# Kernel optimization log

Measured on AMD Instinct MI355X. Metric: run time of the kernel, lower is better.

Reference implementation:

```python
import jax, jax.numpy as jnp
import numpy as np
from jax import lax

B, C, H, W = 2, 256, 64, 64
KC, RD = C // 8, C // 16  # key_channels=32, GatherExcite rd_channels=16
EPS = 1e-5


def setup_inputs() -> dict:
    key = jax.random.key(0)
    ks = jax.random.split(key, 17)
    s = 0.05
    n = lambda k, shp: jax.random.normal(k, shp, jnp.float32) * s
    return {
        "x": jax.random.normal(ks[0], (B, C, H, W), jnp.float32),
        "Wq": n(ks[1], (KC, C)),
        "Wk": n(ks[2], (KC, C)),
        "Wv": n(ks[3], (C, C)),
        "Wb1": n(ks[4], (KC, C)),
        "Wb2": n(ks[5], (KC, C)),
        "w_gb": jax.random.normal(ks[6], (), jnp.float32),  # 1x1 conv on 1-channel bias map
        "ge_w1": n(ks[7], (RD, C)),
        "ge_b1": jnp.zeros((RD,), jnp.float32),
        "ge_w2": n(ks[8], (C, RD)),
        "ge_b2": jnp.zeros((C,), jnp.float32),
        "Wo": n(ks[9], (C, C)),
        "bn_scale": jnp.ones((C,), jnp.float32),
        "bn_bias": jnp.zeros((C,), jnp.float32),
        "bn_mean": jax.random.normal(ks[10], (C,), jnp.float32) * 0.01,
        "bn_var": jnp.ones((C,), jnp.float32),
        "gamma": jax.random.normal(ks[11], (), jnp.float32) * 0.1,
    }


def _conv1x1(t, w):  # t: [B,Cin,H,W], w: [Cout,Cin]
    return jnp.einsum('bchw,oc->bohw', t, w)


def reference(x, Wq, Wk, Wv, Wb1, Wb2, w_gb, ge_w1, ge_b1, ge_w2, ge_b2,
              Wo, bn_scale, bn_bias, bn_mean, bn_var, gamma):
    b, c, h, w = x.shape
    hw = h * w

    # GatherExcite (extent=0, use_mlp=True, gate=sigmoid): global mean -> ConvMlp -> sigmoid gate
    m = x.mean(axis=(2, 3), keepdims=True)                     # [B,C,1,1]
    g = jax.nn.relu(_conv1x1(m, ge_w1) + ge_b1[None, :, None, None])
    g = _conv1x1(g, ge_w2) + ge_b2[None, :, None, None]
    key_in = x * jax.nn.sigmoid(g)                             # [B,C,H,W]

    value = _conv1x1(x, Wv).reshape(b, c, hw).transpose(0, 2, 1)   # [B,HW,C]
    query = _conv1x1(x, Wq).reshape(b, KC, hw).transpose(0, 2, 1)  # [B,HW,Kc]
    key_f = _conv1x1(key_in, Wk).reshape(b, KC, hw)                # [B,Kc,HW]

    sim = jnp.einsum('bnk,bkm->bnm', query, key_f)                 # [B,HW,HW]

    # bias branch (dropout is identity at eval)
    b1 = jax.nn.relu(_conv1x1(x, Wb1)).reshape(b, KC, hw)          # [B,Kc,HW]
    b2 = jax.nn.relu(_conv1x1(x, Wb2)).reshape(b, KC, hw)          # [B,Kc,HW]
    bias = jnp.einsum('bkn,bkm->bnm', b1, b2)                      # [B,HW,HW]

    # AvgPool2d(k=3, s=1, pad=1, count_include_pad=True) on [B,1,HW,HW]
    pooled = lax.reduce_window(bias[:, None], 0.0, lax.add,
                               (1, 1, 3, 3), (1, 1, 1, 1),
                               [(0, 0), (0, 0), (1, 1), (1, 1)]) / 9.0
    bias_map = jax.nn.sigmoid(w_gb * pooled)[:, 0]                 # [B,HW,HW]

    attn = jax.nn.softmax(sim * bias_map, axis=-1)                 # [B,HW,HW]
    ctx = jnp.einsum('bnm,bmc->bnc', attn, value)                  # [B,HW,C]
    ctx = ctx.transpose(0, 2, 1).reshape(b, c, h, w)

    # W: conv1x1 -> BatchNorm (inference) -> ReLU
    y = _conv1x1(ctx, Wo)
    y = (y - bn_mean[None, :, None, None]) * (bn_scale / jnp.sqrt(bn_var + EPS))[None, :, None, None] \
        + bn_bias[None, :, None, None]
    y = jax.nn.relu(y)

    return gamma * y + x
```

## Files before the change

### kernel.cpp

```cpp
#include <hip/hip_runtime.h>
#include <hip/hip_bf16.h>

typedef __bf16 bf16;
typedef __bf16 v8bf __attribute__((ext_vector_type(8)));
typedef __bf16 v4bf __attribute__((ext_vector_type(4)));
typedef float v4f __attribute__((ext_vector_type(4)));

#define HW 4096
#define CH 256
#define KC 32
#define RD 16
#define NB 2
#define BNEPS 1e-5f
#define VSTRIDE 4224
#define LOG2E 1.4426950408889634f

__device__ __forceinline__ float fexp2(float x) {
#if __has_builtin(__builtin_amdgcn_exp2f)
  return __builtin_amdgcn_exp2f(x);
#else
  return exp2f(x);
#endif
}
__device__ __forceinline__ float frcp(float x) {
#if __has_builtin(__builtin_amdgcn_rcpf)
  return __builtin_amdgcn_rcpf(x);
#else
  return 1.f / x;
#endif
}

#define OFF_QT     0u
#define OFF_KT     524288u
#define OFF_BS1    1048576u
#define OFF_BS2    1572864u
#define OFF_VT     2097152u
#define OFF_B1R    6422528u
#define OFF_B2R    6946816u
#define OFF_PACC   7471104u
#define OFF_PL     41025536u
#define OFF_WOBF   41287680u
#define OFF_XBT    41418752u
#define OFF_WALL   45613056u
#define OFF_MPART  46006272u

__global__ __launch_bounds__(256) void k_prep(const float* __restrict__ x,
    bf16* __restrict__ xbt, float* __restrict__ mpart) {
  __shared__ __align__(16) float ts[64][68];
  const int blk = blockIdx.x;
  const int b  = blk >> 8;
  const int id = blk & 255;
  const int ct = id >> 6, nt = id & 63;
  const int c0 = ct * 64, n0 = nt * 64;
  const int t = threadIdx.x;
  const int crow = t >> 2, nch = (t & 3) * 16;
  const float* xp = x + ((size_t)(b * CH + c0 + crow)) * HW + n0 + nch;
  #pragma unroll
  for (int i = 0; i < 4; ++i)
    *(v4f*)&ts[crow][nch + i * 4] = *(const v4f*)(xp + i * 4);
  __syncthreads();
  {
    float p = 0.f;
    #pragma unroll
    for (int j = 0; j < 16; ++j) p += ts[crow][nch + j];
    p += __shfl_xor(p, 1);
    p += __shfl_xor(p, 2);
    if ((t & 3) == 0) mpart[(size_t)(b * CH + c0 + crow) * 64 + nt] = p;
  }
  const int nl = t >> 2, cc0 = (t & 3) * 16;
  bf16* dst = xbt + ((size_t)(b * HW + n0 + nl)) * CH + c0 + cc0;
  v8bf o0, o1;
  #pragma unroll
  for (int j = 0; j < 8; ++j) { o0[j] = (bf16)ts[cc0 + j][nl]; o1[j] = (bf16)ts[cc0 + 8 + j][nl]; }
  *(v8bf*)dst = o0;
  *(v8bf*)(dst + 8) = o1;
}

__global__ __launch_bounds__(256) void k_pack(
    const float* __restrict__ mpart,
    const float* __restrict__ gw1, const float* __restrict__ gb1,
    const float* __restrict__ gw2, const float* __restrict__ gb2,
    const float* __restrict__ Wq, const float* __restrict__ Wk,
    const float* __restrict__ Wb1, const float* __restrict__ Wb2,
    const float* __restrict__ Wv, const float* __restrict__ Wo,
    bf16* __restrict__ wall, bf16* __restrict__ wo_bf) {
  __shared__ float ms[CH];
  __shared__ float hid[RD];
  const int blk = blockIdx.x;
  const int t = threadIdx.x;
  if (blk >= 768) {
    int i = (blk - 768) * 256 + t;
    wo_bf[i] = (bf16)Wo[i];
    return;
  }
  const int b = blk / 384, row = blk % 384;
  float v;
  if (row < 32)       v = Wq[row * CH + t] * LOG2E;
  else if (row < 64) {
    float m = 0.f;
    const float* mp = mpart + (size_t)(b * CH + t) * 64;
    #pragma unroll
    for (int j = 0; j < 64; ++j) m += mp[j];
    ms[t] = m * (1.0f / HW);
    __syncthreads();
    if (t < RD) {
      float a = gb1[t];
      for (int c = 0; c < CH; ++c) a += gw1[t * CH + c] * ms[c];
      hid[t] = fmaxf(a, 0.f);
    }
    __syncthreads();
    float a = gb2[t];
    #pragma unroll
    for (int r = 0; r < RD; ++r) a += gw2[t * RD + r] * hid[r];
    float s = 1.f / (1.f + __expf(-a));
    v = Wk[(row - 32) * CH + t] * s;
  }
  else if (row < 96)  v = Wb1[(row - 64) * CH + t];
  else if (row < 128) v = Wb2[(row - 96) * CH + t];
  else                v = Wv[(row - 128) * CH + t];
  wall[((size_t)b * 384 + row) * CH + t] = (bf16)v;
}

__global__ __launch_bounds__(256, 4) void k_proj(
    const bf16* __restrict__ xbt, const bf16* __restrict__ wall,
    bf16* __restrict__ qt, bf16* __restrict__ kt,
    bf16* __restrict__ b1r, bf16* __restrict__ b2r, bf16* __restrict__ vt) {
  __shared__ __align__(16) bf16 xs[32][264];
  __shared__ __align__(16) bf16 tr[4][16][24];
  const int blk = blockIdx.x;
  const int b  = blk >> 9;
  const int bm = (blk >> 7) & 3;
  const int nt = blk & 127;
  const int n0 = nt * 32;
  const int t = threadIdx.x;
  {
    const int row = t >> 3, c0 = (t & 7) * 32;
    const bf16* src = xbt + ((size_t)(b * HW + n0 + row)) * CH + c0;
    #pragma unroll
    for (int i = 0; i < 4; ++i)
      *(v8bf*)&xs[row][c0 + i * 8] = *(const v8bf*)(src + i * 8);
  }
  __syncthreads();
  const int w = t >> 6, lane = t & 63, cl = lane & 15, kh = lane >> 4;
  const int nsub = (w & 1) * 16;
  const int otrio = (w >> 1) * 3;
  const v4f vzero = {0.f, 0.f, 0.f, 0.f};
  v4f acc[3] = {vzero, vzero, vzero};
  const bf16* wb = wall + ((size_t)b * 384 + bm * 96) * CH;
  for (int kk = 0; kk < 8; ++kk) {
    v8bf bx = *(const v8bf*)&xs[nsub + cl][kk * 32 + kh * 8];
    #pragma unroll
    for (int j = 0; j < 3; ++j) {
      v8bf af = *(const v8bf*)(wb + (size_t)((otrio + j) * 16 + cl) * CH + kk * 32 + kh * 8);
      acc[j] = __builtin_amdgcn_mfma_f32_16x16x32_bf16(af, bx, acc[j], 0, 0, 0);
    }
  }
  const int n = n0 + nsub + cl;
  #pragma unroll
  for (int j = 0; j < 3; ++j) {
    const int o0 = bm * 96 + (otrio + j) * 16;
    if (o0 < 128) {
      const bool rel = (o0 >= 64);
      v4bf pk;
      #pragma unroll
      for (int r = 0; r < 4; ++r) {
        float v = acc[j][r];
        if (rel) v = fmaxf(v, 0.f);
        pk[r] = (bf16)v;
      }
      const int seg = o0 >> 5;
      bf16* base = seg == 0 ? qt : seg == 1 ? kt : seg == 2 ? b1r : b2r;
      *(v4bf*)&base[((size_t)b * HW + n) * KC + (o0 & 31) + kh * 4] = pk;
    } else {
      #pragma unroll
      for (int r = 0; r < 4; ++r) tr[w][kh * 4 + r][cl] = (bf16)acc[j][r];
      asm volatile("s_waitcnt lgkmcnt(0)" ::: "memory");
      __builtin_amdgcn_sched_barrier(0);
      const int row = lane >> 2, nch = (lane & 3) * 4;
      v4bf d = *(const v4bf*)&tr[w][row][nch];
      *(v4bf*)&vt[((size_t)b * CH + (o0 - 128) + row) * VSTRIDE + n0 + nsub + nch] = d;
    }
  }
}

__global__ __launch_bounds__(256) void k_pool(const bf16* __restrict__ b1r,
    const bf16* __restrict__ b2r, const float* __restrict__ wgb,
    bf16* __restrict__ bs1, bf16* __restrict__ bs2) {
  int i = blockIdx.x * 256 + threadIdx.x;
  int n = (i >> 5) & (HW - 1);
  float a = (float)b1r[i], c = (float)b2r[i];
  if (n > 0)      { a += (float)b1r[i - KC]; c += (float)b2r[i - KC]; }
  if (n < HW - 1) { a += (float)b1r[i + KC]; c += (float)b2r[i + KC]; }
  const float ws = -LOG2E * wgb[0] * (1.f / 9.f);
  bs1[i] = (bf16)(a * ws);
  bs2[i] = (bf16)c;
}

__global__ __launch_bounds__(256, 4) void k_attn(
    const bf16* __restrict__ qtg, const bf16* __restrict__ ktg,
    const bf16* __restrict__ bs1g, const bf16* __restrict__ bs2g,
    const bf16* __restrict__ vtg,
    bf16* __restrict__ pacc, float* __restrict__ pl) {
  __shared__ __align__(16) bf16 vbuf[128][64];
  __shared__ __align__(16) bf16 kbuf[2][32][40];
  __shared__ __align__(16) bf16 bbuf[2][32][40];
  __shared__ __align__(16) bf16 plds[2][64][40];
  const int blk = blockIdx.x;
  const int rt  = blk >> 3;
  const int os  = blk & 7;
  const int b   = rt >> 6;
  const int row0 = (rt & 63) * 64;
  const int t = threadIdx.x;
  const int w = t >> 6;
  const int lane = t & 63;
  const int cl = lane & 15, kh = lane >> 4;
  const int kb = os * 512;
  const v4f vzero = {0.f, 0.f, 0.f, 0.f};
  const size_t qoff = ((size_t)(b * HW + row0 + w * 16 + cl)) * KC + kh * 8;
  const v8bf qf  = *(const v8bf*)(qtg + qoff);
  const v8bf b1f = *(const v8bf*)(bs1g + qoff);
  const bf16* kt = ktg + (size_t)b * HW * KC;
  const bf16* b2 = bs2g + (size_t)b * HW * KC;
  const bf16* vt = vtg + (size_t)b * CH * VSTRIDE;
  const int sr = (t >> 2) & 31, sl = (t & 3) * 8;
  const bf16* sbase = (t < 128) ? kt : b2;
  bf16* sd0 = (t < 128) ? &kbuf[0][sr][sl] : &bbuf[0][sr][sl];
  bf16* sd1 = (t < 128) ? &kbuf[1][sr][sl] : &bbuf[1][sr][sl];
  const int vsl = lane & 3;
  const int vslot3 = ((((lane >> 2) & 1) * 4 + vsl) ^ (lane >> 3)) * 8;
  const int rline = w * 32 + (cl >> 1);
  const int rslot = ((((cl & 1) * 4) + kh) ^ (cl >> 1)) * 8;

  *(v8bf*)sd0 = *(const v8bf*)(sbase + (size_t)(kb + sr) * KC + sl);
  __syncthreads();

  v4f acc[16];
  #pragma unroll
  for (int f = 0; f < 16; ++f) acc[f] = vzero;
  float psum = 0.f;

  for (int s = 0; s < 16; ++s) {
    const int m0 = kb + s * 32;
    const int pb = s & 1;
    v8bf vr[4];
    #pragma unroll
    for (int i = 0; i < 4; ++i)
      vr[i] = *(const v8bf*)(vt + (size_t)(w * 64 + i * 16 + (lane >> 2)) * VSTRIDE + m0 + vsl * 8);
    v8bf pr;
    if (s < 15)
      pr = *(const v8bf*)(sbase + (size_t)(m0 + 32 + sr) * KC + sl);
    #pragma unroll
    for (int cb = 0; cb < 2; ++cb) {
      v8bf kf  = *(const v8bf*)&kbuf[pb][cb * 16 + cl][kh * 8];
      v8bf b2f = *(const v8bf*)&bbuf[pb][cb * 16 + cl][kh * 8];
      v4f sim = __builtin_amdgcn_mfma_f32_16x16x32_bf16(kf,  qf,  vzero, 0, 0, 0);
      v4f bia = __builtin_amdgcn_mfma_f32_16x16x32_bf16(b2f, b1f, vzero, 0, 0, 0);
      v4bf pk;
      #pragma unroll
      for (int r = 0; r < 4; ++r) {
        float bm = frcp(1.f + fexp2(bia[r]));
        float pv = fexp2(sim[r] * bm);
        psum += pv;
        pk[r] = (bf16)pv;
      }
      *(v4bf*)&plds[pb][w * 16 + cl][cb * 16 + kh * 4] = pk;
    }
    #pragma unroll
    for (int i = 0; i < 4; ++i)
      *(v8bf*)&vbuf[w * 32 + i * 8 + (lane >> 3)][vslot3] = vr[i];
    if (s < 15) {
      bf16* sd = pb ? sd0 : sd1;
      *(v8bf*)sd = pr;
    }
    __syncthreads();
    v8bf vf[4], pa[4];
    #pragma unroll
    for (int f = 0; f < 4; ++f)
      vf[f] = *(const v8bf*)&vbuf[rline + f * 8][rslot];
    #pragma unroll
    for (int rg = 0; rg < 4; ++rg)
      pa[rg] = *(const v8bf*)&plds[pb][rg * 16 + cl][kh * 8];
    #pragma unroll
    for (int rg = 0; rg < 4; ++rg)
      #pragma unroll
      for (int f = 0; f < 4; ++f)
        acc[rg * 4 + f] = __builtin_amdgcn_mfma_f32_16x16x32_bf16(pa[rg], vf[f], acc[rg * 4 + f], 0, 0, 0);
  }
  __syncthreads();

  {
    float s2 = psum;
    s2 += __shfl_xor(s2, 16);
    s2 += __shfl_xor(s2, 32);
    if (kh == 0) pl[blk * 64 + w * 16 + cl] = s2;
  }
  bf16 (*ep)[64] = (bf16 (*)[64])vbuf;
  bf16* po = pacc + (size_t)blk * 64 * CH;
  for (int rg = 0; rg < 4; ++rg) {
    #pragma unroll
    for (int f = 0; f < 4; ++f)
      #pragma unroll
      for (int r = 0; r < 4; ++r)
        ep[w * 16 + kh * 4 + r][f * 16 + cl] = (bf16)acc[rg * 4 + f][r];
    asm volatile("s_waitcnt lgkmcnt(0)" ::: "memory");
    __builtin_amdgcn_sched_barrier(0);
    #pragma unroll
    for (int it = 0; it < 2; ++it) {
      int row = lane >> 2, chunk = it * 4 + (lane & 3);
      v8bf d = *(const v8bf*)&ep[w * 16 + row][chunk * 8];
      *(v8bf*)&po[(size_t)(rg * 16 + row) * CH + w * 64 + chunk * 8] = d;
    }
  }
}

__global__ __launch_bounds__(256) void k_outc(
    const bf16* __restrict__ pacc, const float* __restrict__ pl,
    const bf16* __restrict__ wo,
    const float* __restrict__ bns, const float* __restrict__ bnb,
    const float* __restrict__ bnm, const float* __restrict__ bnv,
    const float* __restrict__ gamma, const float* __restrict__ x,
    float* __restrict__ out) {
  __shared__ __align__(16) bf16 cs[16][264];
  const int blk = blockIdx.x;
  const int n0g = blk * 16;
  const int b   = n0g >> 12;
  const int n0  = n0g & (HW - 1);
  const int t = threadIdx.x;
  const int base = (blk >> 2) * 8;
  {
    const int r16 = t >> 4;
    const int ch0 = (t & 15) * 16;
    const int rl = (blk & 3) * 16 + r16;
    float den = 0.f;
    #pragma unroll
    for (int s = 0; s < 8; ++s) den += pl[(base + s) * 64 + rl];
    const float inv = 1.f / den;
    float sum[16];
    #pragma unroll
    for (int j = 0; j < 16; ++j) sum[j] = 0.f;
    #pragma unroll
    for (int s = 0; s < 8; ++s) {
      const bf16* pp = &pacc[((size_t)(base + s) * 64 + rl) * CH + ch0];
      v8bf p0 = *(const v8bf*)pp;
      v8bf p1 = *(const v8bf*)(pp + 8);
      #pragma unroll
      for (int j = 0; j < 8; ++j) { sum[j] += (float)p0[j]; sum[8 + j] += (float)p1[j]; }
    }
    v8bf o0, o1;
    #pragma unroll
    for (int j = 0; j < 8; ++j) {
      o0[j] = (bf16)(sum[j] * inv);
      o1[j] = (bf16)(sum[8 + j] * inv);
    }
    *(v8bf*)&cs[r16][ch0] = o0;
    *(v8bf*)&cs[r16][ch0 + 8] = o1;
  }
  __syncthreads();
  const int w = t >> 6, lane = t & 63, cl = lane & 15, kh = lane >> 4;
  const v4f vzero = {0.f, 0.f, 0.f, 0.f};
  v8bf a[8];
  #pragma unroll
  for (int kk = 0; kk < 8; ++kk)
    a[kk] = *(const v8bf*)&cs[cl][kk * 32 + kh * 8];
  v4f acc[4] = {vzero, vzero, vzero, vzero};
  #pragma unroll
  for (int kk = 0; kk < 8; ++kk)
    #pragma unroll
    for (int cg = 0; cg < 4; ++cg) {
      v8bf bfr = *(const v8bf*)(wo + (size_t)(w * 64 + cg * 16 + cl) * CH + kk * 32 + kh * 8);
      acc[cg] = __builtin_amdgcn_mfma_f32_16x16x32_bf16(a[kk], bfr, acc[cg], 0, 0, 0);
    }
  const float g = gamma[0];
  #pragma unroll
  for (int cg = 0; cg < 4; ++cg) {
    int o = w * 64 + cg * 16 + cl;
    float isc = bns[o] / sqrtf(bnv[o] + BNEPS);
    float mu = bnm[o], bb = bnb[o];
    size_t oi = ((size_t)b * CH + o) * HW + n0 + kh * 4;
    v4f xv = *(const v4f*)&x[oi];
    v4f ov;
    #pragma unroll
    for (int r = 0; r < 4; ++r) {
      float v = (acc[cg][r] - mu) * isc + bb;
      v = fmaxf(v, 0.f);
      ov[r] = g * v + xv[r];
    }
    *(v4f*)&out[oi] = ov;
  }
}

extern "C" void kernel_launch(void* const* d_in, const int* in_sizes, int n_in,
                              void* d_out, int out_size, void* d_ws, size_t ws_size,
                              hipStream_t stream) {
  const float* x    = (const float*)d_in[0];
  const float* Wq   = (const float*)d_in[1];
  const float* Wk   = (const float*)d_in[2];
  const float* Wv   = (const float*)d_in[3];
  const float* Wb1  = (const float*)d_in[4];
  const float* Wb2  = (const float*)d_in[5];
  const float* wgb  = (const float*)d_in[6];
  const float* gw1  = (const float*)d_in[7];
  const float* gb1  = (const float*)d_in[8];
  const float* gw2  = (const float*)d_in[9];
  const float* gb2  = (const float*)d_in[10];
  const float* Wo   = (const float*)d_in[11];
  const float* bns  = (const float*)d_in[12];
  const float* bnb  = (const float*)d_in[13];
  const float* bnm  = (const float*)d_in[14];
  const float* bnv  = (const float*)d_in[15];
  const float* gam  = (const float*)d_in[16];

  char* ws = (char*)d_ws;
  bf16* qt    = (bf16*)(ws + OFF_QT);
  bf16* kt    = (bf16*)(ws + OFF_KT);
  bf16* bs1   = (bf16*)(ws + OFF_BS1);
  bf16* bs2   = (bf16*)(ws + OFF_BS2);
  bf16* vt    = (bf16*)(ws + OFF_VT);
  bf16* b1r   = (bf16*)(ws + OFF_B1R);
  bf16* b2r   = (bf16*)(ws + OFF_B2R);
  bf16* pacc  = (bf16*)(ws + OFF_PACC);
  float* plv  = (float*)(ws + OFF_PL);
  bf16* wobf  = (bf16*)(ws + OFF_WOBF);
  bf16* xbt   = (bf16*)(ws + OFF_XBT);
  bf16* wall  = (bf16*)(ws + OFF_WALL);
  float* mprt = (float*)(ws + OFF_MPART);
  float* out  = (float*)d_out;

  hipLaunchKernelGGL(k_prep, dim3(512),  dim3(256), 0, stream, x, xbt, mprt);
  hipLaunchKernelGGL(k_pack, dim3(1024), dim3(256), 0, stream, mprt, gw1, gb1, gw2, gb2,
                     Wq, Wk, Wb1, Wb2, Wv, Wo, wall, wobf);
  hipLaunchKernelGGL(k_proj, dim3(1024), dim3(256), 0, stream, xbt, wall, qt, kt, b1r, b2r, vt);
  hipLaunchKernelGGL(k_pool, dim3(NB * HW * KC / 256), dim3(256), 0, stream, b1r, b2r, wgb, bs1, bs2);
  hipLaunchKernelGGL(k_attn, dim3(1024), dim3(256), 0, stream, qt, kt, bs1, bs2, vt, pacc, plv);
  hipLaunchKernelGGL(k_outc, dim3(512),  dim3(256), 0, stream, pacc, plv, wobf, bns, bnb, bnm, bnv, gam, x, out);
}
```

Baseline: 88.19 us.

## Fuse bias pooling into projection and attention loads, prefetch V one step ahead

Removes the separate k_pool kernel. The w_gb scale is folded into the b1 projection epilogue, and the 3-tap row sums of b1/b2 are computed on the fly while loading into the attention kernel. The attention loop now register-prefetches the next V tile and the next K/B tiles a full iteration ahead, uses a lighter barrier macro, and raises wave priority around the MFMA block. This saves a kernel launch and a global round trip, at the cost of extra redundant loads and adds inside the attention kernel, plus more register pressure.

```diff
diff --git a/kernel.cpp b/kernel.cpp
--- a/kernel.cpp
+++ b/kernel.cpp
@@ -30,12 +30,16 @@
 #endif
 }
 
+#define BLOCK_SYNC() do {                                   \
+  asm volatile("s_waitcnt lgkmcnt(0)" ::: "memory");        \
+  __builtin_amdgcn_s_barrier();                             \
+  __builtin_amdgcn_sched_barrier(0);                        \
+} while (0)
+
 #define OFF_QT     0u
 #define OFF_KT     524288u
-#define OFF_BS1    1048576u
-#define OFF_BS2    1572864u
 #define OFF_VT     2097152u
-#define OFF_B1R    6422528u
+#define OFF_B1S    6422528u
 #define OFF_B2R    6946816u
 #define OFF_PACC   7471104u
 #define OFF_PL     41025536u
@@ -123,8 +127,9 @@
 
 __global__ __launch_bounds__(256, 4) void k_proj(
     const bf16* __restrict__ xbt, const bf16* __restrict__ wall,
+    const float* __restrict__ wgb,
     bf16* __restrict__ qt, bf16* __restrict__ kt,
-    bf16* __restrict__ b1r, bf16* __restrict__ b2r, bf16* __restrict__ vt) {
+    bf16* __restrict__ b1s, bf16* __restrict__ b2r, bf16* __restrict__ vt) {
   __shared__ __align__(16) bf16 xs[32][264];
   __shared__ __align__(16) bf16 tr[4][16][24];
   const int blk = blockIdx.x;
@@ -155,21 +160,22 @@
       acc[j] = __builtin_amdgcn_mfma_f32_16x16x32_bf16(af, bx, acc[j], 0, 0, 0);
     }
   }
+  const float ws = -LOG2E * wgb[0] * (1.f / 9.f);
   const int n = n0 + nsub + cl;
   #pragma unroll
   for (int j = 0; j < 3; ++j) {
     const int o0 = bm * 96 + (otrio + j) * 16;
     if (o0 < 128) {
-      const bool rel = (o0 >= 64);
+      const int seg = o0 >> 5;
       v4bf pk;
       #pragma unroll
       for (int r = 0; r < 4; ++r) {
         float v = acc[j][r];
-        if (rel) v = fmaxf(v, 0.f);
+        if (seg == 2)      v = ws * fmaxf(v, 0.f);
+        else if (seg == 3) v = fmaxf(v, 0.f);
         pk[r] = (bf16)v;
       }
-      const int seg = o0 >> 5;
-      bf16* base = seg == 0 ? qt : seg == 1 ? kt : seg == 2 ? b1r : b2r;
+      bf16* base = seg == 0 ? qt : seg == 1 ? kt : seg == 2 ? b1s : b2r;
       *(v4bf*)&base[((size_t)b * HW + n) * KC + (o0 & 31) + kh * 4] = pk;
     } else {
       #pragma unroll
@@ -183,22 +189,9 @@
   }
 }
 
-__global__ __launch_bounds__(256) void k_pool(const bf16* __restrict__ b1r,
-    const bf16* __restrict__ b2r, const float* __restrict__ wgb,
-    bf16* __restrict__ bs1, bf16* __restrict__ bs2) {
-  int i = blockIdx.x * 256 + threadIdx.x;
-  int n = (i >> 5) & (HW - 1);
-  float a = (float)b1r[i], c = (float)b2r[i];
-  if (n > 0)      { a += (float)b1r[i - KC]; c += (float)b2r[i - KC]; }
-  if (n < HW - 1) { a += (float)b1r[i + KC]; c += (float)b2r[i + KC]; }
-  const float ws = -LOG2E * wgb[0] * (1.f / 9.f);
-  bs1[i] = (bf16)(a * ws);
-  bs2[i] = (bf16)c;
-}
-
 __global__ __launch_bounds__(256, 4) void k_attn(
     const bf16* __restrict__ qtg, const bf16* __restrict__ ktg,
-    const bf16* __restrict__ bs1g, const bf16* __restrict__ bs2g,
+    const bf16* __restrict__ b1sg, const bf16* __restrict__ b2rg,
     const bf16* __restrict__ vtg,
     bf16* __restrict__ pacc, float* __restrict__ pl) {
   __shared__ __align__(16) bf16 vbuf[128][64];
@@ -216,22 +209,53 @@
   const int cl = lane & 15, kh = lane >> 4;
   const int kb = os * 512;
   const v4f vzero = {0.f, 0.f, 0.f, 0.f};
-  const size_t qoff = ((size_t)(b * HW + row0 + w * 16 + cl)) * KC + kh * 8;
-  const v8bf qf  = *(const v8bf*)(qtg + qoff);
-  const v8bf b1f = *(const v8bf*)(bs1g + qoff);
   const bf16* kt = ktg + (size_t)b * HW * KC;
-  const bf16* b2 = bs2g + (size_t)b * HW * KC;
+  const bf16* b2 = b2rg + (size_t)b * HW * KC;
   const bf16* vt = vtg + (size_t)b * CH * VSTRIDE;
+  const int qrow = row0 + w * 16 + cl;
+  const v8bf qf = *(const v8bf*)(qtg + ((size_t)(b * HW + qrow)) * KC + kh * 8);
+  v8bf b1f;
+  {
+    const bf16* bp = b1sg + (size_t)b * HW * KC;
+    v8bf c0 = *(const v8bf*)(bp + (size_t)qrow * KC + kh * 8);
+    v8bf cm = *(const v8bf*)(bp + (size_t)(qrow > 0 ? qrow - 1 : 0) * KC + kh * 8);
+    v8bf cp = *(const v8bf*)(bp + (size_t)(qrow < HW - 1 ? qrow + 1 : HW - 1) * KC + kh * 8);
+    #pragma unroll
+    for (int j = 0; j < 8; ++j) {
+      float sv = (float)c0[j];
+      if (qrow > 0)      sv += (float)cm[j];
+      if (qrow < HW - 1) sv += (float)cp[j];
+      b1f[j] = (bf16)sv;
+    }
+  }
   const int sr = (t >> 2) & 31, sl = (t & 3) * 8;
-  const bf16* sbase = (t < 128) ? kt : b2;
-  bf16* sd0 = (t < 128) ? &kbuf[0][sr][sl] : &bbuf[0][sr][sl];
-  bf16* sd1 = (t < 128) ? &kbuf[1][sr][sl] : &bbuf[1][sr][sl];
+  const bool isK = (t < 128);
   const int vsl = lane & 3;
   const int vslot3 = ((((lane >> 2) & 1) * 4 + vsl) ^ (lane >> 3)) * 8;
   const int rline = w * 32 + (cl >> 1);
   const int rslot = ((((cl & 1) * 4) + kh) ^ (cl >> 1)) * 8;
 
-  *(v8bf*)sd0 = *(const v8bf*)(sbase + (size_t)(kb + sr) * KC + sl);
+  if (isK) {
+    *(v8bf*)&kbuf[0][sr][sl] = *(const v8bf*)(kt + (size_t)(kb + sr) * KC + sl);
+  } else {
+    int g = kb + sr;
+    v8bf c0 = *(const v8bf*)(b2 + (size_t)g * KC + sl);
+    v8bf cm = *(const v8bf*)(b2 + (size_t)(g > 0 ? g - 1 : 0) * KC + sl);
+    v8bf cp = *(const v8bf*)(b2 + (size_t)(g < HW - 1 ? g + 1 : HW - 1) * KC + sl);
+    v8bf o;
+    #pragma unroll
+    for (int j = 0; j < 8; ++j) {
+      float sv = (float)c0[j];
+      if (g > 0)      sv += (float)cm[j];
+      if (g < HW - 1) sv += (float)cp[j];
+      o[j] = (bf16)sv;
+    }
+    *(v8bf*)&bbuf[0][sr][sl] = o;
+  }
+  v8bf vcur[4];
+  #pragma unroll
+  for (int i = 0; i < 4; ++i)
+    vcur[i] = *(const v8bf*)(vt + (size_t)(w * 64 + i * 16 + (lane >> 2)) * VSTRIDE + kb + vsl * 8);
   __syncthreads();
 
   v4f acc[16];
@@ -239,16 +263,24 @@
   for (int f = 0; f < 16; ++f) acc[f] = vzero;
   float psum = 0.f;
 
+  #pragma unroll 2
   for (int s = 0; s < 16; ++s) {
     const int m0 = kb + s * 32;
     const int pb = s & 1;
-    v8bf vr[4];
-    #pragma unroll
-    for (int i = 0; i < 4; ++i)
-      vr[i] = *(const v8bf*)(vt + (size_t)(w * 64 + i * 16 + (lane >> 2)) * VSTRIDE + m0 + vsl * 8);
-    v8bf pr;
-    if (s < 15)
-      pr = *(const v8bf*)(sbase + (size_t)(m0 + 32 + sr) * KC + sl);
+    v8bf kr0, br0, br1, br2, vn[4];
+    if (s < 15) {
+      const int g = m0 + 32 + sr;
+      if (isK) {
+        kr0 = *(const v8bf*)(kt + (size_t)g * KC + sl);
+      } else {
+        br1 = *(const v8bf*)(b2 + (size_t)g * KC + sl);
+        br0 = *(const v8bf*)(b2 + (size_t)(g - 1) * KC + sl);
+        br2 = *(const v8bf*)(b2 + (size_t)(g < HW - 1 ? g + 1 : HW - 1) * KC + sl);
+      }
+      #pragma unroll
+      for (int i = 0; i < 4; ++i)
+        vn[i] = *(const v8bf*)(vt + (size_t)(w * 64 + i * 16 + (lane >> 2)) * VSTRIDE + m0 + 32 + vsl * 8);
+    }
     #pragma unroll
     for (int cb = 0; cb < 2; ++cb) {
       v8bf kf  = *(const v8bf*)&kbuf[pb][cb * 16 + cl][kh * 8];
@@ -265,14 +297,25 @@
       }
       *(v4bf*)&plds[pb][w * 16 + cl][cb * 16 + kh * 4] = pk;
     }
+    if (s < 15) {
+      if (isK) {
+        *(v8bf*)&kbuf[pb ^ 1][sr][sl] = kr0;
+      } else {
+        const int g = m0 + 32 + sr;
+        v8bf o;
+        #pragma unroll
+        for (int j = 0; j < 8; ++j) {
+          float sv = (float)br1[j] + (float)br0[j];
+          if (g < HW - 1) sv += (float)br2[j];
+          o[j] = (bf16)sv;
+        }
+        *(v8bf*)&bbuf[pb ^ 1][sr][sl] = o;
+      }
+    }
     #pragma unroll
     for (int i = 0; i < 4; ++i)
-      *(v8bf*)&vbuf[w * 32 + i * 8 + (lane >> 3)][vslot3] = vr[i];
-    if (s < 15) {
-      bf16* sd = pb ? sd0 : sd1;
-      *(v8bf*)sd = pr;
-    }
-    __syncthreads();
+      *(v8bf*)&vbuf[w * 32 + i * 8 + (lane >> 3)][vslot3] = vcur[i];
+    BLOCK_SYNC();
     v8bf vf[4], pa[4];
     #pragma unroll
     for (int f = 0; f < 4; ++f)
@@ -280,11 +323,17 @@
     #pragma unroll
     for (int rg = 0; rg < 4; ++rg)
       pa[rg] = *(const v8bf*)&plds[pb][rg * 16 + cl][kh * 8];
+    __builtin_amdgcn_s_setprio(1);
     #pragma unroll
     for (int rg = 0; rg < 4; ++rg)
       #pragma unroll
       for (int f = 0; f < 4; ++f)
         acc[rg * 4 + f] = __builtin_amdgcn_mfma_f32_16x16x32_bf16(pa[rg], vf[f], acc[rg * 4 + f], 0, 0, 0);
+    __builtin_amdgcn_s_setprio(0);
+    if (s < 15) {
+      #pragma unroll
+      for (int i = 0; i < 4; ++i) vcur[i] = vn[i];
+    }
   }
   __syncthreads();
 
@@ -413,10 +462,8 @@
   char* ws = (char*)d_ws;
   bf16* qt    = (bf16*)(ws + OFF_QT);
   bf16* kt    = (bf16*)(ws + OFF_KT);
-  bf16* bs1   = (bf16*)(ws + OFF_BS1);
-  bf16* bs2   = (bf16*)(ws + OFF_BS2);
   bf16* vt    = (bf16*)(ws + OFF_VT);
-  bf16* b1r   = (bf16*)(ws + OFF_B1R);
+  bf16* b1s   = (bf16*)(ws + OFF_B1S);
   bf16* b2r   = (bf16*)(ws + OFF_B2R);
   bf16* pacc  = (bf16*)(ws + OFF_PACC);
   float* plv  = (float*)(ws + OFF_PL);
@@ -429,8 +476,7 @@
   hipLaunchKernelGGL(k_prep, dim3(512),  dim3(256), 0, stream, x, xbt, mprt);
   hipLaunchKernelGGL(k_pack, dim3(1024), dim3(256), 0, stream, mprt, gw1, gb1, gw2, gb2,
                      Wq, Wk, Wb1, Wb2, Wv, Wo, wall, wobf);
-  hipLaunchKernelGGL(k_proj, dim3(1024), dim3(256), 0, stream, xbt, wall, qt, kt, b1r, b2r, vt);
-  hipLaunchKernelGGL(k_pool, dim3(NB * HW * KC / 256), dim3(256), 0, stream, b1r, b2r, wgb, bs1, bs2);
-  hipLaunchKernelGGL(k_attn, dim3(1024), dim3(256), 0, stream, qt, kt, bs1, bs2, vt, pacc, plv);
+  hipLaunchKernelGGL(k_proj, dim3(1024), dim3(256), 0, stream, xbt, wall, wgb, qt, kt, b1s, b2r, vt);
+  hipLaunchKernelGGL(k_attn, dim3(1024), dim3(256), 0, stream, qt, kt, b1s, b2r, vt, pacc, plv);
   hipLaunchKernelGGL(k_outc, dim3(512),  dim3(256), 0, stream, pacc, plv, wobf, bns, bnb, bnm, bnv, gam, x, out);
 }
```

Result: slower. 339.5 us (+284.9%).
